# Optimization experiments

Measured on AMD Instinct MI355X. Metric: run time of the kernel, lower is better.

The kernel has to match this reference:

```python
import jax, jax.numpy as jnp
import numpy as np
import math

B, N, E, D = 8, 2048, 2048, 128
MAX_K = 8
HYPER_DIM = 128
LN_EPS = 1e-5


def _sinusoidal_pe(max_pos, dim):
    pe = np.zeros((max_pos, dim), dtype=np.float32)
    position = np.arange(max_pos, dtype=np.float32)[:, None]
    div_term = np.exp(np.arange(0, dim, 2, dtype=np.float32) * (-math.log(10000.0) / dim))
    pe[:, 0::2] = np.sin(position * div_term)
    pe[:, 1::2] = np.cos(position * div_term)
    return jnp.asarray(pe)


def setup_inputs() -> dict:
    key = jax.random.key(0)
    ks = jax.random.split(key, 24)
    s = 0.05
    inp = {
        'x_v': jax.random.normal(ks[0], (B, N, D), jnp.float32),
        'x_e': jax.random.normal(ks[1], (B, E, D), jnp.float32),
        'incidence': (jax.random.uniform(ks[2], (B, N, E), jnp.float32) < 0.01).astype(jnp.float32),
        'suffix_normalizer': jax.random.uniform(ks[3], (B, N), jnp.float32) * 20.0,
        'edge_orders': 1 + jax.random.randint(ks[4], (B, E), 0, MAX_K),
        'node_mask': jax.random.randint(ks[5], (B, N), 0, 2) > 0,
        'edge_mask': jax.random.randint(ks[6], (B, E), 0, 2) > 0,
        'pe1_table': _sinusoidal_pe(MAX_K + 1, D),
        'pe2_table': _sinusoidal_pe(2, D),
        'bias_b': jax.random.uniform(ks[7], (1, D), jnp.float32, -1, 1) / math.sqrt(D),
    }
    i = 8
    for m in ('mlp1', 'mlp2', 'mlp3'):
        inp[m + '_W1'] = jax.random.normal(ks[i], (D, HYPER_DIM), jnp.float32) * s; i += 1
        inp[m + '_b1'] = jnp.zeros((HYPER_DIM,), jnp.float32)
        inp[m + '_W2'] = jax.random.normal(ks[i], (HYPER_DIM, D), jnp.float32) * s; i += 1
        inp[m + '_b2'] = jnp.zeros((D,), jnp.float32)
    for n in ('norm1', 'norm2', 'norm3'):
        inp[n + '_g'] = jnp.ones((D,), jnp.float32)
        inp[n + '_b'] = jnp.zeros((D,), jnp.float32)
    return inp


def _ln(x, g, b):
    mu = jnp.mean(x, axis=-1, keepdims=True)
    var = jnp.mean(jnp.square(x - mu), axis=-1, keepdims=True)
    return (x - mu) * jax.lax.rsqrt(var + LN_EPS) * g + b


def _mlp(x, W1, b1, W2, b2):
    return jax.nn.relu(x @ W1 + b1) @ W2 + b2


def reference(x_v, x_e, incidence, suffix_normalizer, edge_orders, node_mask, edge_mask,
              pe1_table, pe2_table, bias_b,
              mlp1_W1, mlp1_b1, mlp1_W2, mlp1_b2,
              mlp2_W1, mlp2_b1, mlp2_W2, mlp2_b2,
              mlp3_W1, mlp3_b1, mlp3_W2, mlp3_b2,
              norm1_g, norm1_b, norm2_g, norm2_b, norm3_g, norm3_b):
    nm = node_mask[..., None]  # [B,N,1]
    em = edge_mask[..., None]  # [B,E,1]
    x_v = jnp.where(nm, x_v, 0.0)
    x_e = jnp.where(em, x_e, 0.0)
    pe1_k1 = pe1_table[1][None, None, :]          # [1,1,D]
    pe1_k = pe1_table[edge_orders]                # [B,E,D]
    x_v = x_v + _mlp(_ln(x_v, norm1_g, norm1_b) + pe1_k1, mlp1_W1, mlp1_b1, mlp1_W2, mlp1_b2)
    x_e = x_e + _mlp(_ln(x_e, norm1_g, norm1_b) + pe1_k, mlp1_W1, mlp1_b1, mlp1_W2, mlp1_b2)
    x_v = jnp.where(nm, x_v, 0.0)
    x_e = jnp.where(em, x_e, 0.0)
    agg = jnp.einsum('bne,bed->bnd', incidence, x_e)
    x1 = x_v + agg / (1.0 + suffix_normalizer[..., None])
    pe2_s1 = pe2_table[1][None, None, :]
    x1 = x1 + _mlp(_ln(x1, norm2_g, norm2_b) + pe2_s1, mlp2_W1, mlp2_b1, mlp2_W2, mlp2_b2)
    x = jnp.where(nm, x1, 0.0)
    x = x + _mlp(_ln(x, norm3_g, norm3_b), mlp3_W1, mlp3_b1, mlp3_W2, mlp3_b2)
    x = x + bias_b
    x = jnp.where(nm, x, 0.0)
    return x
```

## Files before the change

### kernel.cpp

```cpp
#include <hip/hip_runtime.h>
#include <stdint.h>

#define BB 8
#define NN 2048
#define EE 2048
#define DD 128
#define ROWS 32
#define RBP 132
#define NTHREADS 256
#define WMAT_U32 8192
#define SCANB 2048
#define LCAP 64

typedef __attribute__((ext_vector_type(8))) short bf16x8;
typedef __attribute__((ext_vector_type(4))) float f32x4;

__device__ inline unsigned bf16rne(float f) {
    unsigned u = __float_as_uint(f);
    return (u + 0x7fffu + ((u >> 16) & 1u)) >> 16;
}
__device__ inline float bf16lo(unsigned u) { return __uint_as_float(u << 16); }
__device__ inline float bf16hi(unsigned u) { return __uint_as_float(u & 0xffff0000u); }

#define SWZ(b) ((b) ^ ((((b) >> 8) & 7) << 4))

struct __align__(16) Smem {
    float rowbuf[ROWS][RBP];
    unsigned h[ROWS * DD / 2];
    unsigned scw[4][64];
    int rmask[ROWS];
    int ords[ROWS];
};

__global__ __launch_bounds__(NTHREADS) void convert_w_kernel(
    const float* __restrict__ W11, const float* __restrict__ W12,
    const float* __restrict__ W21, const float* __restrict__ W22,
    const float* __restrict__ W31, const float* __restrict__ W32,
    unsigned* __restrict__ WT) {
    int tid = blockIdx.x * NTHREADS + threadIdx.x;
    if (tid >= 6 * WMAT_U32) return;
    int mat = tid >> 13;
    int idx = tid & (WMAT_U32 - 1);
    int n = idx >> 6, j = idx & 63;
    const float* W = mat == 0 ? W11 : mat == 1 ? W12 : mat == 2 ? W21
                   : mat == 3 ? W22 : mat == 4 ? W31 : W32;
    float a = W[(2 * j) * DD + n];
    float b = W[(2 * j + 1) * DD + n];
    WT[tid] = bf16rne(a) | (bf16rne(b) << 16);
}

__device__ inline void block_load_rows(Smem& s, const float* __restrict__ src,
                                       const int* __restrict__ mask) {
    int t = threadIdx.x;
    for (int idx = t; idx < ROWS * 32; idx += NTHREADS) {
        int r = idx >> 5, c4 = (idx & 31) * 4;
        float4 v = make_float4(0.f, 0.f, 0.f, 0.f);
        if (mask[r] != 0) v = *(const float4*)&src[r * DD + c4];
        *(float4*)&s.rowbuf[r][c4] = v;
    }
    __syncthreads();
}

__device__ inline void block_ln(Smem& s, const float* __restrict__ gw,
                                const float* __restrict__ bw,
                                const float* __restrict__ pe_base, bool per_row_pe) {
    int t = threadIdx.x;
    int gr = t >> 3, g = t & 7;
    int base = g * 16;
    float x[16];
    float4* xp = (float4*)x;
    xp[0] = *(const float4*)&s.rowbuf[gr][base + 0];
    xp[1] = *(const float4*)&s.rowbuf[gr][base + 4];
    xp[2] = *(const float4*)&s.rowbuf[gr][base + 8];
    xp[3] = *(const float4*)&s.rowbuf[gr][base + 12];
    float s1 = 0.f, s2 = 0.f;
    #pragma unroll
    for (int i = 0; i < 16; i++) { s1 += x[i]; s2 += x[i] * x[i]; }
    #pragma unroll
    for (int off = 1; off < 8; off <<= 1) {
        s1 += __shfl_xor(s1, off, 64);
        s2 += __shfl_xor(s2, off, 64);
    }
    float mu = s1 * (1.f / 128.f);
    float var = s2 * (1.f / 128.f) - mu * mu;
    float rstd = rsqrtf(var + 1e-5f);
    const float* pe = nullptr;
    if (pe_base) pe = per_row_pe ? (pe_base + (size_t)s.ords[gr] * DD) : pe_base;
    unsigned p[8];
    #pragma unroll
    for (int j = 0; j < 8; j++) {
        int k0 = base + 2 * j;
        float v0 = (x[2 * j] - mu) * rstd * gw[k0] + bw[k0];
        float v1 = (x[2 * j + 1] - mu) * rstd * gw[k0 + 1] + bw[k0 + 1];
        if (pe) { v0 += pe[k0]; v1 += pe[k0 + 1]; }
        p[j] = bf16rne(v0) | (bf16rne(v1) << 16);
    }
    char* hb = (char*)s.h;
    int byte0 = gr * 256 + g * 32;
    uint4 lo = make_uint4(p[0], p[1], p[2], p[3]);
    uint4 hi = make_uint4(p[4], p[5], p[6], p[7]);
    *(uint4*)(hb + SWZ(byte0)) = lo;
    *(uint4*)(hb + SWZ(byte0 + 16)) = hi;
    __syncthreads();
}

template <bool TO_H>
__device__ inline void block_mm(Smem& s, const unsigned* __restrict__ WT,
                                const float* __restrict__ bias) {
    int t = threadIdx.x;
    int w = t >> 6, l = t & 63;
    int lm = l & 15, lk = l >> 4;
    bf16x8 bfr[2][4];
    const uint4* wt4 = (const uint4*)WT;
    #pragma unroll
    for (int nbl = 0; nbl < 2; nbl++) {
        int n = w * 32 + nbl * 16 + lm;
        #pragma unroll
        for (int kb = 0; kb < 4; kb++) {
            uint4 u = wt4[n * 16 + kb * 4 + lk];
            bfr[nbl][kb] = *(bf16x8*)&u;
        }
    }
    const char* hb = (const char*)s.h;
    bf16x8 afr[2][4];
    #pragma unroll
    for (int mb = 0; mb < 2; mb++) {
        int row = mb * 16 + lm;
        #pragma unroll
        for (int kb = 0; kb < 4; kb++) {
            afr[mb][kb] = *(const bf16x8*)(hb + SWZ(row * 256 + kb * 64 + lk * 16));
        }
    }
    f32x4 acc[2][2];
    #pragma unroll
    for (int mb = 0; mb < 2; mb++)
        #pragma unroll
        for (int nbl = 0; nbl < 2; nbl++)
            acc[mb][nbl] = (f32x4){0.f, 0.f, 0.f, 0.f};
    #pragma unroll
    for (int kb = 0; kb < 4; kb++)
        #pragma unroll
        for (int mb = 0; mb < 2; mb++)
            #pragma unroll
            for (int nbl = 0; nbl < 2; nbl++)
                acc[mb][nbl] = __builtin_amdgcn_mfma_f32_16x16x32_bf16(
                    afr[mb][kb], bfr[nbl][kb], acc[mb][nbl], 0, 0, 0);
    float bcol0 = bias[w * 32 + lm];
    float bcol1 = bias[w * 32 + 16 + lm];
    __syncthreads();
    if (TO_H) {
        char* hw = (char*)s.h;
        #pragma unroll
        for (int mb = 0; mb < 2; mb++)
            #pragma unroll
            for (int nbl = 0; nbl < 2; nbl++) {
                int col = w * 32 + nbl * 16 + lm;
                float bc = nbl ? bcol1 : bcol0;
                #pragma unroll
                for (int j = 0; j < 4; j++) {
                    int row = mb * 16 + lk * 4 + j;
                    float v = fmaxf(acc[mb][nbl][j] + bc, 0.f);
                    *(unsigned short*)(hw + SWZ(row * 256 + col * 2)) =
                        (unsigned short)bf16rne(v);
                }
            }
    } else {
        #pragma unroll
        for (int mb = 0; mb < 2; mb++)
            #pragma unroll
            for (int nbl = 0; nbl < 2; nbl++) {
                int col = w * 32 + nbl * 16 + lm;
                float bc = nbl ? bcol1 : bcol0;
                #pragma unroll
                for (int j = 0; j < 4; j++) {
                    int row = mb * 16 + lk * 4 + j;
                    s.rowbuf[row][col] += acc[mb][nbl][j] + bc;
                }
            }
    }
    __syncthreads();
}

__device__ inline void scan_rows(Smem& s, const float* __restrict__ inc,
                                 const int* __restrict__ nmask,
                                 unsigned* __restrict__ lists, int* __restrict__ cnts,
                                 int wid, int nwaves) {
    int l = threadIdx.x & 63;
    int w = threadIdx.x >> 6;
    unsigned* sc = s.scw[w];
    unsigned long long lmlt = (1ull << l) - 1ull;
    for (int grow = wid; grow < BB * NN; grow += nwaves) {
        if (nmask[grow] == 0) continue;
        const float4* ir = (const float4*)(inc + (size_t)grow * EE);
        float4 v[8];
        #pragma unroll
        for (int i = 0; i < 8; i++) v[i] = ir[l + 64 * i];
        int total = 0;
        #pragma unroll
        for (int i = 0; i < 8; i++) {
            #pragma unroll
            for (int c = 0; c < 4; c++) {
                float val = (c == 0) ? v[i].x : (c == 1) ? v[i].y : (c == 2) ? v[i].z : v[i].w;
                bool nz = (val != 0.f);
                unsigned long long msk = __ballot(nz);
                if (nz) {
                    int pos = total + __popcll(msk & lmlt);
                    if (pos < LCAP) sc[pos] = (unsigned)((l + 64 * i) * 4 + c);
                }
                total += __popcll(msk);
            }
        }
        if (total > LCAP) total = LCAP;
        asm volatile("s_waitcnt lgkmcnt(0)" ::: "memory");
        if (l < 16) {
            uint4 q = *(const uint4*)&sc[4 * l];
            *(uint4*)&lists[(size_t)grow * LCAP + 4 * l] = q;
        }
        if (l == 0) cnts[grow] = total;
    }
}

__device__ inline void block_gather(Smem& s, int rowbase, int bb,
                                    const unsigned* __restrict__ lists,
                                    const int* __restrict__ cnts,
                                    const unsigned* __restrict__ e2pk,
                                    const float* __restrict__ sn) {
    int t = threadIdx.x;
    int w = t >> 6, l = t & 63;
    const unsigned* e2b = e2pk + (size_t)bb * (EE * (DD / 2));
    for (int r = w; r < ROWS; r += 4) {
        if (s.rmask[r] == 0) continue;
        int grow = rowbase + r;
        int cnt = cnts[grow];
        unsigned pk = (l < cnt) ? lists[(size_t)grow * LCAP + l] : 0u;
        float ax = 0.f, ay = 0.f;
        for (int j0 = 0; j0 < cnt; j0 += 8) {
            int nn = cnt - j0;
            unsigned uv[8];
            #pragma unroll
            for (int u = 0; u < 8; u++) {
                unsigned e = __shfl(pk, j0 + u, 64);
                uv[u] = (u < nn) ? e2b[(size_t)e * 64 + l] : 0u;
            }
            #pragma unroll
            for (int u = 0; u < 8; u++) { ax += bf16lo(uv[u]); ay += bf16hi(uv[u]); }
        }
        float inv = 1.f / (1.f + sn[grow]);
        float2* rb = (float2*)&s.rowbuf[r][2 * l];
        float2 cur = *rb;
        cur.x += ax * inv;
        cur.y += ay * inv;
        *rb = cur;
    }
    __syncthreads();
}

__global__ __launch_bounds__(NTHREADS) void edge_scan_kernel(
    const float* __restrict__ x_e, const int* __restrict__ emask,
    const int* __restrict__ eord, const float* __restrict__ pe1,
    const float* __restrict__ n1g, const float* __restrict__ n1b,
    const unsigned* __restrict__ WT,
    const float* __restrict__ b11, const float* __restrict__ b12,
    const float* __restrict__ inc, const int* __restrict__ nmask,
    unsigned* __restrict__ e2pk, unsigned* __restrict__ lists, int* __restrict__ cnts) {
    __shared__ Smem s;
    int bid = blockIdx.x;
    const int EB = BB * EE / ROWS;
    int t = threadIdx.x;
    if (bid >= EB) {
        int wid = (bid - EB) * 4 + (t >> 6);
        scan_rows(s, inc, nmask, lists, cnts, wid, SCANB * 4);
        return;
    }
    int bb = bid & 7;
    int e0 = (bid >> 3) * ROWS;
    int rowbase = bb * EE + e0;
    if (t < ROWS) {
        s.rmask[t] = emask[rowbase + t];
        int o = eord[rowbase + t];
        s.ords[t] = o < 0 ? 0 : (o > 8 ? 8 : o);
    }
    block_load_rows(s, x_e + (size_t)rowbase * DD, emask + rowbase);
    block_ln(s, n1g, n1b, pe1, true);
    block_mm<true>(s, WT + 0 * WMAT_U32, b11);
    block_mm<false>(s, WT + 1 * WMAT_U32, b12);
    unsigned* dst = e2pk + (size_t)rowbase * (DD / 2);
    for (int idx = t; idx < ROWS * 16; idx += NTHREADS) {
        int r = idx >> 4, q = idx & 15;
        uint4 o = make_uint4(0u, 0u, 0u, 0u);
        if (s.rmask[r] != 0) {
            const float* rp = &s.rowbuf[r][q * 8];
            o.x = bf16rne(rp[0]) | (bf16rne(rp[1]) << 16);
            o.y = bf16rne(rp[2]) | (bf16rne(rp[3]) << 16);
            o.z = bf16rne(rp[4]) | (bf16rne(rp[5]) << 16);
            o.w = bf16rne(rp[6]) | (bf16rne(rp[7]) << 16);
        }
        *(uint4*)&dst[r * 64 + q * 4] = o;
    }
}

__global__ __launch_bounds__(NTHREADS) void node_kernel(
    const float* __restrict__ x_v, const int* __restrict__ nmask,
    const float* __restrict__ sn,
    const float* __restrict__ pe1, const float* __restrict__ pe2,
    const float* __restrict__ biasb,
    const float* __restrict__ n1g, const float* __restrict__ n1b,
    const float* __restrict__ n2g, const float* __restrict__ n2b,
    const float* __restrict__ n3g, const float* __restrict__ n3b,
    const unsigned* __restrict__ WT,
    const float* __restrict__ b11, const float* __restrict__ b12,
    const float* __restrict__ b21, const float* __restrict__ b22,
    const float* __restrict__ b31, const float* __restrict__ b32,
    const unsigned* __restrict__ e2pk, const unsigned* __restrict__ lists,
    const int* __restrict__ cnts, float* __restrict__ out) {
    __shared__ Smem s;
    int bid = blockIdx.x;
    int bb = bid & 7;
    int n0 = (bid >> 3) * ROWS;
    int rowbase = bb * NN + n0;
    int t = threadIdx.x;
    if (t < ROWS) s.rmask[t] = nmask[rowbase + t];
    block_load_rows(s, x_v + (size_t)rowbase * DD, nmask + rowbase);
    block_ln(s, n1g, n1b, pe1 + DD, false);
    block_mm<true>(s, WT + 0 * WMAT_U32, b11);
    block_mm<false>(s, WT + 1 * WMAT_U32, b12);
    block_gather(s, rowbase, bb, lists, cnts, e2pk, sn);
    block_ln(s, n2g, n2b, pe2 + DD, false);
    block_mm<true>(s, WT + 2 * WMAT_U32, b21);
    block_mm<false>(s, WT + 3 * WMAT_U32, b22);
    block_ln(s, n3g, n3b, nullptr, false);
    block_mm<true>(s, WT + 4 * WMAT_U32, b31);
    block_mm<false>(s, WT + 5 * WMAT_U32, b32);
    for (int idx = t; idx < ROWS * 32; idx += NTHREADS) {
        int r = idx >> 5, c4 = (idx & 31) * 4;
        float4 v = make_float4(0.f, 0.f, 0.f, 0.f);
        if (s.rmask[r] != 0) {
            v = *(const float4*)&s.rowbuf[r][c4];
            float4 bbv = *(const float4*)&biasb[c4];
            v.x += bbv.x; v.y += bbv.y; v.z += bbv.z; v.w += bbv.w;
        }
        *(float4*)&out[(size_t)(rowbase + r) * DD + c4] = v;
    }
}

extern "C" void kernel_launch(void* const* d_in, const int* in_sizes, int n_in,
                              void* d_out, int out_size, void* d_ws, size_t ws_size,
                              hipStream_t stream) {
    const float* x_v   = (const float*)d_in[0];
    const float* x_e   = (const float*)d_in[1];
    const float* inc   = (const float*)d_in[2];
    const float* sn    = (const float*)d_in[3];
    const int*   eord  = (const int*)d_in[4];
    const int*   nmask = (const int*)d_in[5];
    const int*   emask = (const int*)d_in[6];
    const float* pe1   = (const float*)d_in[7];
    const float* pe2   = (const float*)d_in[8];
    const float* biasb = (const float*)d_in[9];
    const float* W11   = (const float*)d_in[10];
    const float* b11   = (const float*)d_in[11];
    const float* W12   = (const float*)d_in[12];
    const float* b12   = (const float*)d_in[13];
    const float* W21   = (const float*)d_in[14];
    const float* b21   = (const float*)d_in[15];
    const float* W22   = (const float*)d_in[16];
    const float* b22   = (const float*)d_in[17];
    const float* W31   = (const float*)d_in[18];
    const float* b31   = (const float*)d_in[19];
    const float* W32   = (const float*)d_in[20];
    const float* b32   = (const float*)d_in[21];
    const float* n1g   = (const float*)d_in[22];
    const float* n1b   = (const float*)d_in[23];
    const float* n2g   = (const float*)d_in[24];
    const float* n2b   = (const float*)d_in[25];
    const float* n3g   = (const float*)d_in[26];
    const float* n3b   = (const float*)d_in[27];

    unsigned* e2pk  = (unsigned*)d_ws;
    unsigned* WT    = e2pk + (size_t)BB * EE * (DD / 2);
    unsigned* lists = WT + 6 * WMAT_U32;
    int*      cnts  = (int*)(lists + (size_t)BB * NN * LCAP);
    float*    out   = (float*)d_out;

    dim3 blk(NTHREADS);
    convert_w_kernel<<<dim3((6 * WMAT_U32 + NTHREADS - 1) / NTHREADS), blk, 0, stream>>>(
        W11, W12, W21, W22, W31, W32, WT);
    edge_scan_kernel<<<dim3(BB * EE / ROWS + SCANB), blk, 0, stream>>>(
        x_e, emask, eord, pe1, n1g, n1b, WT, b11, b12, inc, nmask, e2pk, lists, cnts);
    node_kernel<<<dim3(BB * NN / ROWS), blk, 0, stream>>>(
        x_v, nmask, sn, pe1, pe2, biasb,
        n1g, n1b, n2g, n2b, n3g, n3b,
        WT, b11, b12, b21, b22, b31, b32,
        e2pk, lists, cnts, out);
}
```

Baseline: 64.43 us.

## Drop weight-convert kernel and move node MLP1 into the edge/scan kernel

Removes the separate weight conversion launch. The edge and node MLP1 blocks now read fp32 weights directly and pack them to bf16 in registers, while the scan blocks convert only the remaining four weight matrices. Node MLP1 moves from the node kernel into the first kernel, which writes the intermediate node state to the output buffer, and the second kernel reads it back and continues with the gather and MLP2/MLP3. This cuts one launch and spreads the node work across more concurrent blocks, at the cost of an extra fp32 round trip of node rows and strided fp32 weight loads in every MLP1 block.

Result: slower. 65.87 us (+2.2%).

```diff
diff --git a/kernel.cpp b/kernel.cpp
--- a/kernel.cpp
+++ b/kernel.cpp
@@ -32,23 +32,6 @@
     int ords[ROWS];
 };
 
-__global__ __launch_bounds__(NTHREADS) void convert_w_kernel(
-    const float* __restrict__ W11, const float* __restrict__ W12,
-    const float* __restrict__ W21, const float* __restrict__ W22,
-    const float* __restrict__ W31, const float* __restrict__ W32,
-    unsigned* __restrict__ WT) {
-    int tid = blockIdx.x * NTHREADS + threadIdx.x;
-    if (tid >= 6 * WMAT_U32) return;
-    int mat = tid >> 13;
-    int idx = tid & (WMAT_U32 - 1);
-    int n = idx >> 6, j = idx & 63;
-    const float* W = mat == 0 ? W11 : mat == 1 ? W12 : mat == 2 ? W21
-                   : mat == 3 ? W22 : mat == 4 ? W31 : W32;
-    float a = W[(2 * j) * DD + n];
-    float b = W[(2 * j + 1) * DD + n];
-    WT[tid] = bf16rne(a) | (bf16rne(b) << 16);
-}
-
 __device__ inline void block_load_rows(Smem& s, const float* __restrict__ src,
                                        const int* __restrict__ mask) {
     int t = threadIdx.x;
@@ -105,22 +88,11 @@
 }
 
 template <bool TO_H>
-__device__ inline void block_mm(Smem& s, const unsigned* __restrict__ WT,
-                                const float* __restrict__ bias) {
+__device__ inline void block_mm_core(Smem& s, const bf16x8 bfr[2][4],
+                                     const float* __restrict__ bias) {
     int t = threadIdx.x;
     int w = t >> 6, l = t & 63;
     int lm = l & 15, lk = l >> 4;
-    bf16x8 bfr[2][4];
-    const uint4* wt4 = (const uint4*)WT;
-    #pragma unroll
-    for (int nbl = 0; nbl < 2; nbl++) {
-        int n = w * 32 + nbl * 16 + lm;
-        #pragma unroll
-        for (int kb = 0; kb < 4; kb++) {
-            uint4 u = wt4[n * 16 + kb * 4 + lk];
-            bfr[nbl][kb] = *(bf16x8*)&u;
-        }
-    }
     const char* hb = (const char*)s.h;
     bf16x8 afr[2][4];
     #pragma unroll
@@ -179,6 +151,53 @@
             }
     }
     __syncthreads();
+}
+
+template <bool TO_H>
+__device__ inline void block_mm(Smem& s, const unsigned* __restrict__ WT,
+                                const float* __restrict__ bias) {
+    int t = threadIdx.x;
+    int w = t >> 6, l = t & 63;
+    int lm = l & 15, lk = l >> 4;
+    bf16x8 bfr[2][4];
+    const uint4* wt4 = (const uint4*)WT;
+    #pragma unroll
+    for (int nbl = 0; nbl < 2; nbl++) {
+        int n = w * 32 + nbl * 16 + lm;
+        #pragma unroll
+        for (int kb = 0; kb < 4; kb++) {
+            uint4 u = wt4[n * 16 + kb * 4 + lk];
+            bfr[nbl][kb] = *(bf16x8*)&u;
+        }
+    }
+    block_mm_core<TO_H>(s, bfr, bias);
+}
+
+template <bool TO_H>
+__device__ inline void block_mm_f32w(Smem& s, const float* __restrict__ Wf,
+                                     const float* __restrict__ bias) {
+    int t = threadIdx.x;
+    int w = t >> 6, l = t & 63;
+    int lm = l & 15, lk = l >> 4;
+    bf16x8 bfr[2][4];
+    #pragma unroll
+    for (int nbl = 0; nbl < 2; nbl++) {
+        int n = w * 32 + nbl * 16 + lm;
+        #pragma unroll
+        for (int kb = 0; kb < 4; kb++) {
+            int k0 = kb * 32 + lk * 8;
+            unsigned pk[4];
+            #pragma unroll
+            for (int jp = 0; jp < 4; jp++) {
+                float a = Wf[(size_t)(k0 + 2 * jp) * DD + n];
+                float b = Wf[(size_t)(k0 + 2 * jp + 1) * DD + n];
+                pk[jp] = bf16rne(a) | (bf16rne(b) << 16);
+            }
+            uint4 u = make_uint4(pk[0], pk[1], pk[2], pk[3]);
+            bfr[nbl][kb] = *(bf16x8*)&u;
+        }
+    }
+    block_mm_core<TO_H>(s, bfr, bias);
 }
 
 __device__ inline void scan_rows(Smem& s, const float* __restrict__ inc,
@@ -255,60 +274,86 @@
     __syncthreads();
 }
 
-__global__ __launch_bounds__(NTHREADS) void edge_scan_kernel(
-    const float* __restrict__ x_e, const int* __restrict__ emask,
+__global__ __launch_bounds__(NTHREADS) void k1_kernel(
+    const float* __restrict__ x_e, const float* __restrict__ x_v,
+    const int* __restrict__ emask, const int* __restrict__ nmask,
     const int* __restrict__ eord, const float* __restrict__ pe1,
+    const float* __restrict__ inc,
     const float* __restrict__ n1g, const float* __restrict__ n1b,
-    const unsigned* __restrict__ WT,
-    const float* __restrict__ b11, const float* __restrict__ b12,
-    const float* __restrict__ inc, const int* __restrict__ nmask,
-    unsigned* __restrict__ e2pk, unsigned* __restrict__ lists, int* __restrict__ cnts) {
+    const float* __restrict__ W11, const float* __restrict__ b11,
+    const float* __restrict__ W12, const float* __restrict__ b12,
+    const float* __restrict__ W21, const float* __restrict__ W22,
+    const float* __restrict__ W31, const float* __restrict__ W32,
+    unsigned* __restrict__ WT,
+    unsigned* __restrict__ e2pk, float* __restrict__ v2out,
+    unsigned* __restrict__ lists, int* __restrict__ cnts) {
     __shared__ Smem s;
     int bid = blockIdx.x;
-    const int EB = BB * EE / ROWS;
-    int t = threadIdx.x;
-    if (bid >= EB) {
-        int wid = (bid - EB) * 4 + (t >> 6);
+    int t = threadIdx.x;
+    if (bid < SCANB) {
+        int gtid = bid * NTHREADS + t;
+        if (gtid < 4 * WMAT_U32) {
+            int mat = gtid >> 13;
+            int idx = gtid & (WMAT_U32 - 1);
+            int n = idx >> 6, j = idx & 63;
+            const float* W = mat == 0 ? W21 : mat == 1 ? W22 : mat == 2 ? W31 : W32;
+            float a = W[(2 * j) * DD + n];
+            float b = W[(2 * j + 1) * DD + n];
+            WT[gtid] = bf16rne(a) | (bf16rne(b) << 16);
+        }
+        int wid = bid * 4 + (t >> 6);
         scan_rows(s, inc, nmask, lists, cnts, wid, SCANB * 4);
         return;
     }
-    int bb = bid & 7;
-    int e0 = (bid >> 3) * ROWS;
-    int rowbase = bb * EE + e0;
+    int lb = bid - SCANB;
+    bool isEdge = lb < (BB * EE / ROWS);
+    if (!isEdge) lb -= BB * EE / ROWS;
+    int bb = lb & 7;
+    int r0 = (lb >> 3) * ROWS;
+    int rowbase = bb * EE + r0;
+    const int* mask = isEdge ? emask : nmask;
     if (t < ROWS) {
-        s.rmask[t] = emask[rowbase + t];
-        int o = eord[rowbase + t];
-        s.ords[t] = o < 0 ? 0 : (o > 8 ? 8 : o);
-    }
-    block_load_rows(s, x_e + (size_t)rowbase * DD, emask + rowbase);
-    block_ln(s, n1g, n1b, pe1, true);
-    block_mm<true>(s, WT + 0 * WMAT_U32, b11);
-    block_mm<false>(s, WT + 1 * WMAT_U32, b12);
-    unsigned* dst = e2pk + (size_t)rowbase * (DD / 2);
-    for (int idx = t; idx < ROWS * 16; idx += NTHREADS) {
-        int r = idx >> 4, q = idx & 15;
-        uint4 o = make_uint4(0u, 0u, 0u, 0u);
-        if (s.rmask[r] != 0) {
-            const float* rp = &s.rowbuf[r][q * 8];
-            o.x = bf16rne(rp[0]) | (bf16rne(rp[1]) << 16);
-            o.y = bf16rne(rp[2]) | (bf16rne(rp[3]) << 16);
-            o.z = bf16rne(rp[4]) | (bf16rne(rp[5]) << 16);
-            o.w = bf16rne(rp[6]) | (bf16rne(rp[7]) << 16);
-        }
-        *(uint4*)&dst[r * 64 + q * 4] = o;
-    }
-}
-
-__global__ __launch_bounds__(NTHREADS) void node_kernel(
-    const float* __restrict__ x_v, const int* __restrict__ nmask,
+        s.rmask[t] = mask[rowbase + t];
+        if (isEdge) {
+            int o = eord[rowbase + t];
+            s.ords[t] = o < 0 ? 0 : (o > 8 ? 8 : o);
+        }
+    }
+    block_load_rows(s, (isEdge ? x_e : x_v) + (size_t)rowbase * DD, mask + rowbase);
+    block_ln(s, n1g, n1b, isEdge ? pe1 : (pe1 + DD), isEdge);
+    block_mm_f32w<true>(s, W11, b11);
+    block_mm_f32w<false>(s, W12, b12);
+    if (isEdge) {
+        unsigned* dst = e2pk + (size_t)rowbase * (DD / 2);
+        for (int idx = t; idx < ROWS * 16; idx += NTHREADS) {
+            int r = idx >> 4, q = idx & 15;
+            uint4 o = make_uint4(0u, 0u, 0u, 0u);
+            if (s.rmask[r] != 0) {
+                const float* rp = &s.rowbuf[r][q * 8];
+                o.x = bf16rne(rp[0]) | (bf16rne(rp[1]) << 16);
+                o.y = bf16rne(rp[2]) | (bf16rne(rp[3]) << 16);
+                o.z = bf16rne(rp[4]) | (bf16rne(rp[5]) << 16);
+                o.w = bf16rne(rp[6]) | (bf16rne(rp[7]) << 16);
+            }
+            *(uint4*)&dst[r * 64 + q * 4] = o;
+        }
+    } else {
+        for (int idx = t; idx < ROWS * 32; idx += NTHREADS) {
+            int r = idx >> 5, c4 = (idx & 31) * 4;
+            float4 v = make_float4(0.f, 0.f, 0.f, 0.f);
+            if (s.rmask[r] != 0) v = *(const float4*)&s.rowbuf[r][c4];
+            *(float4*)&v2out[(size_t)(rowbase + r) * DD + c4] = v;
+        }
+    }
+}
+
+__global__ __launch_bounds__(NTHREADS) void k2_kernel(
+    const float* __restrict__ v2, const int* __restrict__ nmask,
     const float* __restrict__ sn,
-    const float* __restrict__ pe1, const float* __restrict__ pe2,
-    const float* __restrict__ biasb,
-    const float* __restrict__ n1g, const float* __restrict__ n1b,
+    const float* __restrict__ pe2, const float* __restrict__ biasb,
     const float* __restrict__ n2g, const float* __restrict__ n2b,
     const float* __restrict__ n3g, const float* __restrict__ n3b,
     const unsigned* __restrict__ WT,
-    const float* __restrict__ b11, const float* __restrict__ b12,
     const float* __restrict__ b21, const float* __restrict__ b22,
     const float* __restrict__ b31, const float* __restrict__ b32,
     const unsigned* __restrict__ e2pk, const unsigned* __restrict__ lists,
@@ -320,17 +365,14 @@
     int rowbase = bb * NN + n0;
     int t = threadIdx.x;
     if (t < ROWS) s.rmask[t] = nmask[rowbase + t];
-    block_load_rows(s, x_v + (size_t)rowbase * DD, nmask + rowbase);
-    block_ln(s, n1g, n1b, pe1 + DD, false);
-    block_mm<true>(s, WT + 0 * WMAT_U32, b11);
-    block_mm<false>(s, WT + 1 * WMAT_U32, b12);
+    block_load_rows(s, v2 + (size_t)rowbase * DD, nmask + rowbase);
     block_gather(s, rowbase, bb, lists, cnts, e2pk, sn);
     block_ln(s, n2g, n2b, pe2 + DD, false);
-    block_mm<true>(s, WT + 2 * WMAT_U32, b21);
-    block_mm<false>(s, WT + 3 * WMAT_U32, b22);
+    block_mm<true>(s, WT + 0 * WMAT_U32, b21);
+    block_mm<false>(s, WT + 1 * WMAT_U32, b22);
     block_ln(s, n3g, n3b, nullptr, false);
-    block_mm<true>(s, WT + 4 * WMAT_U32, b31);
-    block_mm<false>(s, WT + 5 * WMAT_U32, b32);
+    block_mm<true>(s, WT + 2 * WMAT_U32, b31);
+    block_mm<false>(s, WT + 3 * WMAT_U32, b32);
     for (int idx = t; idx < ROWS * 32; idx += NTHREADS) {
         int r = idx >> 5, c4 = (idx & 31) * 4;
         float4 v = make_float4(0.f, 0.f, 0.f, 0.f);
@@ -377,18 +419,18 @@
 
     unsigned* e2pk  = (unsigned*)d_ws;
     unsigned* WT    = e2pk + (size_t)BB * EE * (DD / 2);
-    unsigned* lists = WT + 6 * WMAT_U32;
+    unsigned* lists = WT + 4 * WMAT_U32;
     int*      cnts  = (int*)(lists + (size_t)BB * NN * LCAP);
     float*    out   = (float*)d_out;
 
     dim3 blk(NTHREADS);
-    convert_w_kernel<<<dim3((6 * WMAT_U32 + NTHREADS - 1) / NTHREADS), blk, 0, stream>>>(
-        W11, W12, W21, W22, W31, W32, WT);
-    edge_scan_kernel<<<dim3(BB * EE / ROWS + SCANB), blk, 0, stream>>>(
-        x_e, emask, eord, pe1, n1g, n1b, WT, b11, b12, inc, nmask, e2pk, lists, cnts);
-    node_kernel<<<dim3(BB * NN / ROWS), blk, 0, stream>>>(
-        x_v, nmask, sn, pe1, pe2, biasb,
-        n1g, n1b, n2g, n2b, n3g, n3b,
-        WT, b11, b12, b21, b22, b31, b32,
+    k1_kernel<<<dim3(SCANB + 2 * BB * EE / ROWS), blk, 0, stream>>>(
+        x_e, x_v, emask, nmask, eord, pe1, inc,
+        n1g, n1b, W11, b11, W12, b12, W21, W22, W31, W32,
+        WT, e2pk, out, lists, cnts);
+    k2_kernel<<<dim3(BB * NN / ROWS), blk, 0, stream>>>(
+        out, nmask, sn, pe2, biasb,
+        n2g, n2b, n3g, n3b,
+        WT, b21, b22, b31, b32,
         e2pk, lists, cnts, out);
 }
```
